# Kernel optimization log

Hardware: AMD Instinct MI355X
Metric: run time of the kernel (lower is better)

Reference implementation:

```python
import jax, jax.numpy as jnp
import numpy as np

INPUT_DIM = 1024
HEADS = 16
HEAD_DIM = 64
OUT_DIM = HEADS * HEAD_DIM
B, S = 4, 2048


def _xavier(key, shape):
    fan_in, fan_out = shape
    limit = float(np.sqrt(6.0 / (fan_in + fan_out)))
    return jax.random.uniform(key, shape, jnp.float32, -limit, limit)


def setup_inputs() -> dict:
    key = jax.random.key(0)
    kq, kk, kv, kwq, kwk, kwv = jax.random.split(key, 6)
    return {
        "query": jax.random.normal(kq, (B, S, INPUT_DIM), jnp.float32),
        "key": jax.random.normal(kk, (B, S, INPUT_DIM), jnp.float32),
        "value": jax.random.normal(kv, (B, S, INPUT_DIM), jnp.float32),
        "WQ": _xavier(kwq, (INPUT_DIM, OUT_DIM)),
        "WK": _xavier(kwk, (INPUT_DIM, OUT_DIM)),
        "WV": _xavier(kwv, (INPUT_DIM, OUT_DIM)),
    }


def reference(query, key, value, WQ, WK, WV):
    b, s, _ = query.shape
    # Project and split into heads: [B, H, S, D]
    q = (query @ WQ).reshape(b, s, HEADS, HEAD_DIM).transpose(0, 2, 1, 3)
    k = (key @ WK).reshape(b, s, HEADS, HEAD_DIM).transpose(0, 2, 1, 3)
    v = (value @ WV).reshape(b, s, HEADS, HEAD_DIM).transpose(0, 2, 1, 3)
    scores = jnp.einsum("bhqd,bhkd->bhqk", q, k) / jnp.sqrt(
        jnp.asarray(HEAD_DIM, q.dtype)
    )
    attn = jax.nn.softmax(scores, axis=-1)
    out = jnp.einsum("bhqk,bhkd->bhqd", attn, v)
    return out.transpose(0, 2, 1, 3).reshape(b, s, OUT_DIM)
```

## Files before the change

kernel.cpp:

```cpp
#include <hip/hip_runtime.h>
#include <stdint.h>

#define HEADS 16
#define HDIM  64
#define NDIM  1024
#define BATCH 4
#define SEQ   2048
#define MTOT  (BATCH * SEQ)

typedef __attribute__((ext_vector_type(8))) short short8;
typedef __attribute__((ext_vector_type(4))) float float4v;
typedef __attribute__((ext_vector_type(4))) int int4v;
typedef __attribute__((ext_vector_type(2))) int int2v;
typedef __attribute__((ext_vector_type(4))) unsigned short ushort4v;

static __device__ __forceinline__ unsigned int fbits(float f) {
    union { float f; unsigned int u; } v; v.f = f; return v.u;
}
static __device__ __forceinline__ unsigned short bf16r(float f) {
    return (unsigned short)((fbits(f) + 0x8000u) >> 16);
}
static __device__ __forceinline__ unsigned int pack2(float lo, float hi) {
    return ((fbits(hi) + 0x8000u) & 0xffff0000u) | ((fbits(lo) + 0x8000u) >> 16);
}
static __device__ __forceinline__ unsigned int cvt_pk_bf16(float lo, float hi) {
    unsigned int r;
    asm("v_cvt_pk_bf16_f32 %0, %1, %2" : "=v"(r) : "v"(lo), "v"(hi));
    return r;
}

static __device__ __forceinline__ void gl_lds16(const unsigned short* g, unsigned short* l) {
    __builtin_amdgcn_global_load_lds(
        (const __attribute__((address_space(1))) unsigned int*)(uintptr_t)g,
        (__attribute__((address_space(3))) unsigned int*)(uintptr_t)l,
        16, 0, 0);
}

__global__ __launch_bounds__(256) void cast_x(
    const float* __restrict__ X0, const float* __restrict__ X1, const float* __restrict__ X2,
    unsigned short* __restrict__ Y0, unsigned short* __restrict__ Y1, unsigned short* __restrict__ Y2)
{
    int z = blockIdx.z;
    const float* X = (z == 0) ? X0 : (z == 1) ? X1 : X2;
    unsigned short* Y = (z == 0) ? Y0 : (z == 1) ? Y1 : Y2;
    size_t i = ((size_t)blockIdx.x * 256 + threadIdx.x) * 8;
    float4v a = *(const float4v*)(X + i);
    float4v b = *(const float4v*)(X + i + 4);
    int4v p;
    p.x = pack2(a.x, a.y); p.y = pack2(a.z, a.w);
    p.z = pack2(b.x, b.y); p.w = pack2(b.z, b.w);
    *(int4v*)(Y + i) = p;
}

__global__ __launch_bounds__(256) void cast_transpose_w(
    const float* __restrict__ W0, const float* __restrict__ W1, const float* __restrict__ W2,
    unsigned short* __restrict__ T0, unsigned short* __restrict__ T1, unsigned short* __restrict__ T2)
{
    const float* W = (blockIdx.z == 0) ? W0 : (blockIdx.z == 1) ? W1 : W2;
    unsigned short* T = (blockIdx.z == 0) ? T0 : (blockIdx.z == 1) ? T1 : T2;
    __shared__ __align__(16) unsigned short tile[64][65];
    int t = threadIdx.x;
    int k0 = blockIdx.y * 64, n0 = blockIdx.x * 64;
    int row = t >> 2, seg = (t & 3) * 16;
    const float* src = W + (size_t)(k0 + row) * NDIM + n0 + seg;
#pragma unroll
    for (int i = 0; i < 4; ++i) {
        float4v v = *(const float4v*)(src + i * 4);
        tile[row][seg + i*4 + 0] = bf16r(v.x);
        tile[row][seg + i*4 + 1] = bf16r(v.y);
        tile[row][seg + i*4 + 2] = bf16r(v.z);
        tile[row][seg + i*4 + 3] = bf16r(v.w);
    }
    __syncthreads();
    unsigned short* dst = T + (size_t)(n0 + row) * NDIM + k0 + seg;
#pragma unroll
    for (int i = 0; i < 4; ++i) {
        ushort4v o;
        o.x = tile[seg + i*4 + 0][row];
        o.y = tile[seg + i*4 + 1][row];
        o.z = tile[seg + i*4 + 2][row];
        o.w = tile[seg + i*4 + 3][row];
        *(ushort4v*)(dst + i*4) = o;
    }
}

#define BM 128
#define BN 128
#define BK 64

__global__ __launch_bounds__(256) void proj_gemm(
    const unsigned short* __restrict__ Xqc, const unsigned short* __restrict__ Xkc,
    const unsigned short* __restrict__ Xvc,
    const unsigned short* __restrict__ Tq, const unsigned short* __restrict__ Tk, const unsigned short* __restrict__ Tv,
    unsigned short* __restrict__ Oq, unsigned short* __restrict__ Ok, unsigned short* __restrict__ Ov,
    float qscale)
{
    int z = blockIdx.z;
    const unsigned short* Xc = (z == 0) ? Xqc : (z == 1) ? Xkc : Xvc;
    const unsigned short* Wt = (z == 0) ? Tq : (z == 1) ? Tk : Tv;
    unsigned short* Out = (z == 0) ? Oq : (z == 1) ? Ok : Ov;
    float scale = (z == 0) ? qscale : 1.0f;
    bool vtrans = (z == 2);

    __shared__ __align__(16) unsigned short Asm[BM * BK];
    __shared__ __align__(16) unsigned short Bsm[BN * BK];

    int t = threadIdx.x;
    int wave = t >> 6, lane = t & 63, l15 = lane & 15, quad = lane >> 4;
    int m0 = blockIdx.x * BM, n0 = blockIdx.y * BN;
    int wm = (wave >> 1) * 64, wn = (wave & 1) * 64;

    float4v acc[4][4];
#pragma unroll
    for (int i = 0; i < 4; ++i)
#pragma unroll
        for (int j = 0; j < 4; ++j) acc[i][j] = (float4v){0.f, 0.f, 0.f, 0.f};

    const unsigned short* gaP[4];
    const unsigned short* gbP[4];
    unsigned short* asP[4];
    unsigned short* bsP[4];
#pragma unroll
    for (int i = 0; i < 4; ++i) {
        int c = t + i * 256;
        int row = c >> 3;
        int blk = (c & 7) ^ (row & 7);
        gaP[i] = Xc + (size_t)(m0 + row) * NDIM + blk * 8;
        gbP[i] = Wt + (size_t)(n0 + row) * NDIM + blk * 8;
        asP[i] = &Asm[c * 8];
        bsP[i] = &Bsm[c * 8];
    }

    for (int kt = 0; kt < NDIM; kt += BK) {
        __syncthreads();
#pragma unroll
        for (int i = 0; i < 4; ++i) {
            gl_lds16(gaP[i] + kt, asP[i]);
            gl_lds16(gbP[i] + kt, bsP[i]);
        }
        __syncthreads();

#pragma unroll
        for (int ksub = 0; ksub < 2; ++ksub) {
            short8 af[4], bfr[4];
#pragma unroll
            for (int mt = 0; mt < 4; ++mt) {
                int row = wm + mt * 16 + l15;
                af[mt] = *(const short8*)&Asm[row * BK + (((ksub * 4 + quad) ^ (row & 7)) * 8)];
            }
#pragma unroll
            for (int nt = 0; nt < 4; ++nt) {
                int row = wn + nt * 16 + l15;
                bfr[nt] = *(const short8*)&Bsm[row * BK + (((ksub * 4 + quad) ^ (row & 7)) * 8)];
            }
#pragma unroll
            for (int mt = 0; mt < 4; ++mt)
#pragma unroll
                for (int nt = 0; nt < 4; ++nt)
                    acc[mt][nt] = __builtin_amdgcn_mfma_f32_16x16x32_bf16(af[mt], bfr[nt], acc[mt][nt], 0, 0, 0);
        }
    }

#pragma unroll
    for (int mt = 0; mt < 4; ++mt) {
        int mbase = m0 + wm + mt * 16 + quad * 4;
        int b = mbase >> 11;
        int s = mbase & 2047;
#pragma unroll
        for (int nt = 0; nt < 4; ++nt) {
            int gn = n0 + wn + nt * 16 + l15;
            int h = gn >> 6, d = gn & 63;
            if (!vtrans) {
                size_t base = ((size_t)((b * HEADS + h) * SEQ + s)) * HDIM + d;
#pragma unroll
                for (int r = 0; r < 4; ++r)
                    Out[base + (size_t)r * HDIM] = bf16r(acc[mt][nt][r] * scale);
            } else {
                size_t base = ((size_t)((b * HEADS + h) * HDIM + d)) * SEQ + s;
                ushort4v o;
                o.x = bf16r(acc[mt][nt][0]);
                o.y = bf16r(acc[mt][nt][1]);
                o.z = bf16r(acc[mt][nt][2]);
                o.w = bf16r(acc[mt][nt][3]);
                *(ushort4v*)(Out + base) = o;
            }
        }
    }
}

#define BQ  256
#define BKC 64

__global__ __launch_bounds__(256) void attn_kernel(
    const unsigned short* __restrict__ Q,
    const unsigned short* __restrict__ K,
    const unsigned short* __restrict__ Vt,
    float* __restrict__ Out)
{
    __shared__ __align__(16) unsigned short Ksm[BKC][72];
    __shared__ __align__(16) unsigned short Vsm[HDIM][72];
    __shared__ __align__(16) unsigned short Psm[4][64][72];

    int t = threadIdx.x;
    int wave = t >> 6, lane = t & 63, l15 = lane & 15, quad = lane >> 4;
    int L = blockIdx.x;
    int bh = L & 63;
    int b = bh >> 4, h = bh & 15;
    int q0 = (L >> 6) * BQ;

    const unsigned short* Qbh = Q + (size_t)bh * SEQ * HDIM;
    const unsigned short* Kbh = K + (size_t)bh * SEQ * HDIM;
    const unsigned short* Vbh = Vt + (size_t)bh * HDIM * SEQ;

    short8 qf[4][2];
#pragma unroll
    for (int mt = 0; mt < 4; ++mt) {
        int qr = q0 + wave * 64 + mt * 16 + l15;
        qf[mt][0] = *(const short8*)(Qbh + (size_t)qr * HDIM + quad * 8);
        qf[mt][1] = *(const short8*)(Qbh + (size_t)qr * HDIM + 32 + quad * 8);
    }

    float lsum[4][4];
    float4v acc_o[4][4];
#pragma unroll
    for (int mt = 0; mt < 4; ++mt) {
#pragma unroll
        for (int r = 0; r < 4; ++r) lsum[mt][r] = 0.f;
#pragma unroll
        for (int dtt = 0; dtt < 4; ++dtt) acc_o[mt][dtt] = (float4v){0.f, 0.f, 0.f, 0.f};
    }

    int srow = t >> 2;
    int sseg = (t & 3) * 16;
    const unsigned short* kptr = Kbh + (size_t)srow * HDIM + sseg;
    const unsigned short* vptr = Vbh + (size_t)srow * SEQ + sseg;

    short8 kv0 = *(const short8*)(kptr);
    short8 kv1 = *(const short8*)(kptr + 8);
    short8 kv2 = *(const short8*)(vptr);
    short8 kv3 = *(const short8*)(vptr + 8);

    for (int kc = 0; kc < SEQ; kc += BKC) {
        __syncthreads();
        *(short8*)&Ksm[srow][sseg]     = kv0;
        *(short8*)&Ksm[srow][sseg + 8] = kv1;
        *(short8*)&Vsm[srow][sseg]     = kv2;
        *(short8*)&Vsm[srow][sseg + 8] = kv3;
        __syncthreads();

        int kn = kc + BKC;
        if (kn < SEQ) {
            kv0 = *(const short8*)(kptr + (size_t)kn * HDIM);
            kv1 = *(const short8*)(kptr + (size_t)kn * HDIM + 8);
            kv2 = *(const short8*)(vptr + kn);
            kv3 = *(const short8*)(vptr + kn + 8);
        }

        short8 kf[4][2];
#pragma unroll
        for (int nt = 0; nt < 4; ++nt) {
            kf[nt][0] = *(const short8*)&Ksm[l15 * 4 + nt][quad * 8];
            kf[nt][1] = *(const short8*)&Ksm[l15 * 4 + nt][32 + quad * 8];
        }

#pragma unroll
        for (int mt = 0; mt < 4; ++mt) {
            float4v sc[4];
#pragma unroll
            for (int nt = 0; nt < 4; ++nt) sc[nt] = (float4v){0.f, 0.f, 0.f, 0.f};
            __builtin_amdgcn_s_setprio(1);
#pragma unroll
            for (int nt = 0; nt < 4; ++nt) {
                sc[nt] = __builtin_amdgcn_mfma_f32_16x16x32_bf16(qf[mt][0], kf[nt][0], sc[nt], 0, 0, 0);
                sc[nt] = __builtin_amdgcn_mfma_f32_16x16x32_bf16(qf[mt][1], kf[nt][1], sc[nt], 0, 0, 0);
            }
            __builtin_amdgcn_s_setprio(0);

#pragma unroll
            for (int r = 0; r < 4; ++r) {
                float p0 = __builtin_amdgcn_exp2f(sc[0][r]);
                float p1 = __builtin_amdgcn_exp2f(sc[1][r]);
                float p2 = __builtin_amdgcn_exp2f(sc[2][r]);
                float p3 = __builtin_amdgcn_exp2f(sc[3][r]);
                lsum[mt][r] += (p0 + p1) + (p2 + p3);
                int row = mt * 16 + quad * 4 + r;
                int2v pw;
                pw.x = (int)cvt_pk_bf16(p0, p1);
                pw.y = (int)cvt_pk_bf16(p2, p3);
                *(int2v*)&Psm[wave][row][l15 * 4] = pw;
            }
        }

        __builtin_amdgcn_s_setprio(1);
#pragma unroll
        for (int kseg = 0; kseg < 2; ++kseg) {
            short8 pf[4], vf[4];
#pragma unroll
            for (int mt = 0; mt < 4; ++mt)
                pf[mt] = *(const short8*)&Psm[wave][mt * 16 + l15][kseg * 32 + quad * 8];
#pragma unroll
            for (int dtt = 0; dtt < 4; ++dtt)
                vf[dtt] = *(const short8*)&Vsm[dtt * 16 + l15][kseg * 32 + quad * 8];
#pragma unroll
            for (int mt = 0; mt < 4; ++mt)
#pragma unroll
                for (int dtt = 0; dtt < 4; ++dtt)
                    acc_o[mt][dtt] = __builtin_amdgcn_mfma_f32_16x16x32_bf16(pf[mt], vf[dtt], acc_o[mt][dtt], 0, 0, 0);
        }
        __builtin_amdgcn_s_setprio(0);
    }

#pragma unroll
    for (int mt = 0; mt < 4; ++mt)
#pragma unroll
        for (int r = 0; r < 4; ++r) {
            float l = lsum[mt][r];
            l += __shfl_xor(l, 1);
            l += __shfl_xor(l, 2);
            l += __shfl_xor(l, 4);
            l += __shfl_xor(l, 8);
            float inv = 1.0f / l;
            int qrow = q0 + wave * 64 + mt * 16 + quad * 4 + r;
            size_t base = ((size_t)(b * SEQ + qrow)) * NDIM + h * HDIM;
#pragma unroll
            for (int dtt = 0; dtt < 4; ++dtt)
                Out[base + dtt * 16 + l15] = acc_o[mt][dtt][r] * inv;
        }
}

extern "C" void kernel_launch(void* const* d_in, const int* in_sizes, int n_in,
                              void* d_out, int out_size, void* d_ws, size_t ws_size,
                              hipStream_t stream)
{
    const float* q_in = (const float*)d_in[0];
    const float* k_in = (const float*)d_in[1];
    const float* v_in = (const float*)d_in[2];
    const float* WQ = (const float*)d_in[3];
    const float* WK = (const float*)d_in[4];
    const float* WV = (const float*)d_in[5];
    float* out = (float*)d_out;

    unsigned short* ws = (unsigned short*)d_ws;
    size_t wsz = (size_t)NDIM * NDIM;
    size_t psz = (size_t)MTOT * NDIM;
    unsigned short* Tq = ws;
    unsigned short* Tk = Tq + wsz;
    unsigned short* Tv = Tk + wsz;
    unsigned short* Qp = Tv + wsz;
    unsigned short* Kp = Qp + psz;
    unsigned short* Vp = Kp + psz;
    unsigned short* Xvc = Vp + psz;

    unsigned short* Xqc = (unsigned short*)d_out;
    unsigned short* Xkc = Xqc + psz;

    cast_x<<<dim3(MTOT * NDIM / (256 * 8), 1, 3), 256, 0, stream>>>(
        q_in, k_in, v_in, Xqc, Xkc, Xvc);
    cast_transpose_w<<<dim3(16, 16, 3), 256, 0, stream>>>(WQ, WK, WV, Tq, Tk, Tv);
    proj_gemm<<<dim3(MTOT / BM, NDIM / BN, 3), 256, 0, stream>>>(
        Xqc, Xkc, Xvc, Tq, Tk, Tv, Qp, Kp, Vp, 0.125f * 1.44269504088896f);
    attn_kernel<<<dim3(SEQ / BQ * BATCH * HEADS), 256, 0, stream>>>(Qp, Kp, Vp, out);
}
```

Measured before the change: 286.4 us.

## Rewrite projection GEMM as 256x256 8-wave double-buffered pipelined kernel

Replaces the 128x128 single-buffered projection GEMM with a 256x256 tile, 512-thread kernel that double-buffers LDS (128KB dynamic shared memory) and overlaps global-to-LDS loads with MFMA work. It uses explicit barriers, vmcnt waits and setprio to interleave LDS fragment reads with MFMA clusters. The three weights are addressed as one concatenated buffer via Tq, which relies on Tq/Tk/Tv being contiguous in the workspace. The larger tile is meant to raise arithmetic intensity and hide load latency, at the cost of fewer blocks and high register and LDS pressure.

```diff
diff --git a/kernel.cpp b/kernel.cpp
--- a/kernel.cpp
+++ b/kernel.cpp
@@ -84,92 +84,173 @@
     }
 }
 
-#define BM 128
-#define BN 128
-#define BK 64
-
-__global__ __launch_bounds__(256) void proj_gemm(
+#define BK8 64
+
+__global__ __launch_bounds__(512, 2) void proj_gemm8(
     const unsigned short* __restrict__ Xqc, const unsigned short* __restrict__ Xkc,
     const unsigned short* __restrict__ Xvc,
-    const unsigned short* __restrict__ Tq, const unsigned short* __restrict__ Tk, const unsigned short* __restrict__ Tv,
+    const unsigned short* __restrict__ Wall,
     unsigned short* __restrict__ Oq, unsigned short* __restrict__ Ok, unsigned short* __restrict__ Ov,
     float qscale)
 {
-    int z = blockIdx.z;
+    extern __shared__ __align__(16) unsigned short sm[];
+
+    int t = threadIdx.x;
+    int wave = t >> 6, lane = t & 63, l15 = lane & 15, quad = lane >> 4;
+    int m0 = blockIdx.x * 256;
+    int by = blockIdx.y;
+    int n0 = by * 256;
+    int z = by >> 2;
     const unsigned short* Xc = (z == 0) ? Xqc : (z == 1) ? Xkc : Xvc;
-    const unsigned short* Wt = (z == 0) ? Tq : (z == 1) ? Tk : Tv;
     unsigned short* Out = (z == 0) ? Oq : (z == 1) ? Ok : Ov;
     float scale = (z == 0) ? qscale : 1.0f;
     bool vtrans = (z == 2);
 
-    __shared__ __align__(16) unsigned short Asm[BM * BK];
-    __shared__ __align__(16) unsigned short Bsm[BN * BK];
-
-    int t = threadIdx.x;
-    int wave = t >> 6, lane = t & 63, l15 = lane & 15, quad = lane >> 4;
-    int m0 = blockIdx.x * BM, n0 = blockIdx.y * BN;
-    int wm = (wave >> 1) * 64, wn = (wave & 1) * 64;
-
-    float4v acc[4][4];
-#pragma unroll
-    for (int i = 0; i < 4; ++i)
+    int ah = wave >> 2;
+    int bh2 = (wave & 3) >> 1;
+    int brow = ((wave & 3) & 1) * 64;
+
+    int r0 = t >> 3,  b0 = (t & 7) ^ (r0 & 7);
+    int r1 = r0 + 64, b1 = (t & 7) ^ (r1 & 7);
+    const unsigned short* gA0 = Xc   + (size_t)(m0 + r0) * NDIM + b0 * 8;
+    const unsigned short* gA1 = Xc   + (size_t)(m0 + r1) * NDIM + b1 * 8;
+    const unsigned short* gB0 = Wall + (size_t)(n0 + r0) * NDIM + b0 * 8;
+    const unsigned short* gB1 = Wall + (size_t)(n0 + r1) * NDIM + b1 * 8;
+    unsigned short* lA0 = sm + t * 8;
+    unsigned short* lA1 = sm + t * 8 + 4096;
+    unsigned short* lB0 = sm + 16384 + t * 8;
+    unsigned short* lB1 = sm + 16384 + t * 8 + 4096;
+
+#define STAGE8(TK, CUR) do {                                            \
+        int kt_ = (TK) * BK8;                                           \
+        int co_ = (CUR) * 32768;                                        \
+        gl_lds16(gA0 + kt_,          lA0 + co_);                        \
+        gl_lds16(gA1 + kt_,          lA1 + co_);                        \
+        gl_lds16(gA0 + 131072 + kt_, lA0 + co_ + 8192);                 \
+        gl_lds16(gA1 + 131072 + kt_, lA1 + co_ + 8192);                 \
+        gl_lds16(gB0 + kt_,          lB0 + co_);                        \
+        gl_lds16(gB1 + kt_,          lB1 + co_);                        \
+        gl_lds16(gB0 + 131072 + kt_, lB0 + co_ + 8192);                 \
+        gl_lds16(gB1 + 131072 + kt_, lB1 + co_ + 8192);                 \
+    } while (0)
+
+    float4v acc[8][4];
+#pragma unroll
+    for (int i = 0; i < 8; ++i)
 #pragma unroll
         for (int j = 0; j < 4; ++j) acc[i][j] = (float4v){0.f, 0.f, 0.f, 0.f};
 
-    const unsigned short* gaP[4];
-    const unsigned short* gbP[4];
-    unsigned short* asP[4];
-    unsigned short* bsP[4];
-#pragma unroll
-    for (int i = 0; i < 4; ++i) {
-        int c = t + i * 256;
-        int row = c >> 3;
-        int blk = (c & 7) ^ (row & 7);
-        gaP[i] = Xc + (size_t)(m0 + row) * NDIM + blk * 8;
-        gbP[i] = Wt + (size_t)(n0 + row) * NDIM + blk * 8;
-        asP[i] = &Asm[c * 8];
-        bsP[i] = &Bsm[c * 8];
-    }
-
-    for (int kt = 0; kt < NDIM; kt += BK) {
-        __syncthreads();
-#pragma unroll
-        for (int i = 0; i < 4; ++i) {
-            gl_lds16(gaP[i] + kt, asP[i]);
-            gl_lds16(gbP[i] + kt, bsP[i]);
-        }
-        __syncthreads();
-
-#pragma unroll
-        for (int ksub = 0; ksub < 2; ++ksub) {
-            short8 af[4], bfr[4];
-#pragma unroll
-            for (int mt = 0; mt < 4; ++mt) {
-                int row = wm + mt * 16 + l15;
-                af[mt] = *(const short8*)&Asm[row * BK + (((ksub * 4 + quad) ^ (row & 7)) * 8)];
-            }
-#pragma unroll
-            for (int nt = 0; nt < 4; ++nt) {
-                int row = wn + nt * 16 + l15;
-                bfr[nt] = *(const short8*)&Bsm[row * BK + (((ksub * 4 + quad) ^ (row & 7)) * 8)];
-            }
-#pragma unroll
-            for (int mt = 0; mt < 4; ++mt)
-#pragma unroll
-                for (int nt = 0; nt < 4; ++nt)
-                    acc[mt][nt] = __builtin_amdgcn_mfma_f32_16x16x32_bf16(af[mt], bfr[nt], acc[mt][nt], 0, 0, 0);
-        }
-    }
-
-#pragma unroll
-    for (int mt = 0; mt < 4; ++mt) {
-        int mbase = m0 + wm + mt * 16 + quad * 4;
+    STAGE8(0, 0);
+    STAGE8(1, 1);
+    asm volatile("s_waitcnt vmcnt(8)");
+    __builtin_amdgcn_sched_barrier(0);
+    __builtin_amdgcn_s_barrier();
+
+    short8 afr[4][2], bf01[2][2], bf23[2][2];
+
+    for (int tk = 0; tk < 16; ++tk) {
+        int cbase = (tk & 1) * 32768;
+        int aoff = cbase + ah * 8192;
+        int boff = cbase + 16384 + bh2 * 8192;
+
+#pragma unroll
+        for (int mt = 0; mt < 4; ++mt) {
+            int ar = mt * 16 + l15;
+#pragma unroll
+            for (int ks = 0; ks < 2; ++ks)
+                afr[mt][ks] = *(const short8*)&sm[aoff + ar * 64 + (((ks * 4 + quad) ^ (ar & 7)) * 8)];
+        }
+#pragma unroll
+        for (int nt = 0; nt < 2; ++nt) {
+            int br = brow + nt * 16 + l15;
+#pragma unroll
+            for (int ks = 0; ks < 2; ++ks)
+                bf01[nt][ks] = *(const short8*)&sm[boff + br * 64 + (((ks * 4 + quad) ^ (br & 7)) * 8)];
+        }
+        __builtin_amdgcn_s_barrier();
+        asm volatile("s_waitcnt lgkmcnt(0)");
+        __builtin_amdgcn_sched_barrier(0);
+        __builtin_amdgcn_s_setprio(1);
+#pragma unroll
+        for (int mt = 0; mt < 4; ++mt)
+#pragma unroll
+            for (int nt = 0; nt < 2; ++nt)
+#pragma unroll
+                for (int ks = 0; ks < 2; ++ks)
+                    acc[mt][nt] = __builtin_amdgcn_mfma_f32_16x16x32_bf16(afr[mt][ks], bf01[nt][ks], acc[mt][nt], 0, 0, 0);
+        __builtin_amdgcn_s_setprio(0);
+        __builtin_amdgcn_s_barrier();
+
+#pragma unroll
+        for (int nt = 0; nt < 2; ++nt) {
+            int br = brow + (nt + 2) * 16 + l15;
+#pragma unroll
+            for (int ks = 0; ks < 2; ++ks)
+                bf23[nt][ks] = *(const short8*)&sm[boff + br * 64 + (((ks * 4 + quad) ^ (br & 7)) * 8)];
+        }
+        __builtin_amdgcn_s_barrier();
+        asm volatile("s_waitcnt lgkmcnt(0)");
+        __builtin_amdgcn_sched_barrier(0);
+        __builtin_amdgcn_s_setprio(1);
+#pragma unroll
+        for (int mt = 0; mt < 4; ++mt)
+#pragma unroll
+            for (int nt = 0; nt < 2; ++nt)
+#pragma unroll
+                for (int ks = 0; ks < 2; ++ks)
+                    acc[mt][nt + 2] = __builtin_amdgcn_mfma_f32_16x16x32_bf16(afr[mt][ks], bf23[nt][ks], acc[mt][nt + 2], 0, 0, 0);
+        __builtin_amdgcn_s_setprio(0);
+        __builtin_amdgcn_s_barrier();
+
+#pragma unroll
+        for (int mt = 0; mt < 4; ++mt) {
+            int ar = (mt + 4) * 16 + l15;
+#pragma unroll
+            for (int ks = 0; ks < 2; ++ks)
+                afr[mt][ks] = *(const short8*)&sm[aoff + ar * 64 + (((ks * 4 + quad) ^ (ar & 7)) * 8)];
+        }
+        __builtin_amdgcn_s_barrier();
+        asm volatile("s_waitcnt lgkmcnt(0)");
+        __builtin_amdgcn_sched_barrier(0);
+        __builtin_amdgcn_s_setprio(1);
+#pragma unroll
+        for (int mt = 0; mt < 4; ++mt)
+#pragma unroll
+            for (int nt = 0; nt < 2; ++nt)
+#pragma unroll
+                for (int ks = 0; ks < 2; ++ks)
+                    acc[mt + 4][nt] = __builtin_amdgcn_mfma_f32_16x16x32_bf16(afr[mt][ks], bf01[nt][ks], acc[mt + 4][nt], 0, 0, 0);
+        __builtin_amdgcn_s_setprio(0);
+        __builtin_amdgcn_s_barrier();
+
+        if (tk < 14) STAGE8(tk + 2, tk & 1);
+        __builtin_amdgcn_s_barrier();
+        __builtin_amdgcn_s_setprio(1);
+#pragma unroll
+        for (int mt = 0; mt < 4; ++mt)
+#pragma unroll
+            for (int nt = 0; nt < 2; ++nt)
+#pragma unroll
+                for (int ks = 0; ks < 2; ++ks)
+                    acc[mt + 4][nt + 2] = __builtin_amdgcn_mfma_f32_16x16x32_bf16(afr[mt][ks], bf23[nt][ks], acc[mt + 4][nt + 2], 0, 0, 0);
+        __builtin_amdgcn_s_setprio(0);
+        if (tk < 14) { asm volatile("s_waitcnt vmcnt(8)"); }
+        else         { asm volatile("s_waitcnt vmcnt(0)"); }
+        __builtin_amdgcn_sched_barrier(0);
+        __builtin_amdgcn_s_barrier();
+    }
+#undef STAGE8
+
+#pragma unroll
+    for (int mt = 0; mt < 8; ++mt) {
+        int mbase = m0 + ah * 128 + mt * 16 + quad * 4;
         int b = mbase >> 11;
         int s = mbase & 2047;
 #pragma unroll
         for (int nt = 0; nt < 4; ++nt) {
-            int gn = n0 + wn + nt * 16 + l15;
-            int h = gn >> 6, d = gn & 63;
+            int gnl = (wave & 3) * 64 + nt * 16 + l15;
+            int nn = (n0 + gnl) & 1023;
+            int h = nn >> 6, d = nn & 63;
             if (!vtrans) {
                 size_t base = ((size_t)((b * HEADS + h) * SEQ + s)) * HDIM + d;
 #pragma unroll
@@ -357,7 +438,7 @@
     cast_x<<<dim3(MTOT * NDIM / (256 * 8), 1, 3), 256, 0, stream>>>(
         q_in, k_in, v_in, Xqc, Xkc, Xvc);
     cast_transpose_w<<<dim3(16, 16, 3), 256, 0, stream>>>(WQ, WK, WV, Tq, Tk, Tv);
-    proj_gemm<<<dim3(MTOT / BM, NDIM / BN, 3), 256, 0, stream>>>(
-        Xqc, Xkc, Xvc, Tq, Tk, Tv, Qp, Kp, Vp, 0.125f * 1.44269504088896f);
+    proj_gemm8<<<dim3(MTOT / 256, 3 * NDIM / 256), 512, 131072, stream>>>(
+        Xqc, Xkc, Xvc, Tq, Qp, Kp, Vp, 0.125f * 1.44269504088896f);
     attn_kernel<<<dim3(SEQ / BQ * BATCH * HEADS), 256, 0, stream>>>(Qp, Kp, Vp, out);
 }
```

Result: slower. 302.0 us (+5.4%).
